# Kernel tuning notes

Measured on AMD Instinct MI355X. Metric: run time of the kernel, lower is better.

The kernel has to match this reference:

```python
import jax, jax.numpy as jnp
import numpy as np

BN_EPS = 1e-5

def _conv1x1(w, b, x):
    # w: (O, C), b: (O,), x: (B, C, T) -> (B, O, T)
    return jnp.einsum('oc,bct->bot', w, x) + b[None, :, None]

def _maxpool2(x):
    # MaxPool1d(kernel_size=2, stride=2): (B, C, T) -> (B, C, T//2)
    B, C, T = x.shape
    return x.reshape(B, C, T // 2, 2).max(axis=-1)

def setup_inputs() -> dict:
    key = jax.random.key(0)
    ks = jax.random.split(key, 11)
    B, C, Ci, T = 4, 256, 128, 8192
    s_in = 1.0 / np.sqrt(C)
    s_ic = 1.0 / np.sqrt(Ci)
    return {
        'x':       jax.random.normal(ks[0], (B, C, T), dtype=jnp.float32),
        'theta_w': jax.random.uniform(ks[1], (Ci, C), jnp.float32, -s_in, s_in),
        'theta_b': jax.random.uniform(ks[2], (Ci,),   jnp.float32, -s_in, s_in),
        'phi_w':   jax.random.uniform(ks[3], (Ci, C), jnp.float32, -s_in, s_in),
        'phi_b':   jax.random.uniform(ks[4], (Ci,),   jnp.float32, -s_in, s_in),
        'g_w':     jax.random.uniform(ks[5], (Ci, C), jnp.float32, -s_in, s_in),
        'g_b':     jax.random.uniform(ks[6], (Ci,),   jnp.float32, -s_in, s_in),
        'w_w':     jax.random.uniform(ks[7], (C, Ci), jnp.float32, -s_ic, s_ic),
        'w_b':     jax.random.uniform(ks[8], (C,),    jnp.float32, -s_ic, s_ic),
        'gamma':   jax.random.normal(ks[9], (C,), dtype=jnp.float32),
        'beta':    jax.random.normal(ks[10], (C,), dtype=jnp.float32),
    }

def reference(x, theta_w, theta_b, phi_w, phi_b, g_w, g_b, w_w, w_b, gamma, beta):
    # x: (B, C, T)
    theta = _conv1x1(theta_w, theta_b, x)            # (B, Ci, T)
    phi   = _maxpool2(_conv1x1(phi_w, phi_b, x))     # (B, Ci, N), N = T//2
    g     = _maxpool2(_conv1x1(g_w, g_b, x))         # (B, Ci, N)
    N = phi.shape[-1]
    # f = theta^T phi / N  (dot-product similarity, divide-by-N normalization)
    f = jnp.einsum('bct,bcn->btn', theta, phi) / N   # (B, T, N)
    y = jnp.einsum('btn,bcn->bct', f, g)             # (B, Ci, T)
    wy = _conv1x1(w_w, w_b, y)                       # (B, C, T)
    # BatchNorm1d (training mode: batch statistics over (B, T), biased var)
    mean = wy.mean(axis=(0, 2), keepdims=True)
    var = ((wy - mean) ** 2).mean(axis=(0, 2), keepdims=True)
    bn = gamma[None, :, None] * (wy - mean) * jax.lax.rsqrt(var + BN_EPS) + beta[None, :, None]
    return bn + x
```

## Files before the change

kernel.cpp:

```cpp
#include <hip/hip_runtime.h>
#include <hip/hip_bf16.h>


constexpr int B = 4, C = 256, CI = 128, T = 8192, NN = 4096;

using s16x8 = __attribute__((ext_vector_type(8))) short;
using f32x4 = __attribute__((ext_vector_type(4))) float;

__device__ __forceinline__ unsigned short f2bf(float f) {
    unsigned int x = __float_as_uint(f);
    unsigned int r = (x + 0x7fffu + ((x >> 16) & 1u)) >> 16;
    return (unsigned short)r;
}
__device__ __forceinline__ float bf2f(unsigned short u) {
    return __uint_as_float((unsigned int)u << 16);
}

#define MFMA(a, b, c) __builtin_amdgcn_mfma_f32_16x16x32_bf16((a), (b), (c), 0, 0, 0)

constexpr size_t SZ_XT = (size_t)B * T * C * 2;
constexpr size_t O_XTH = 0;
constexpr size_t O_XTL = O_XTH + SZ_XT;
constexpr size_t O_WSH = O_XTL + SZ_XT;
constexpr size_t O_WSL = O_WSH + (size_t)C * C * 2;
constexpr size_t SZ_P  = (size_t)B * CI * NN * 2;
constexpr size_t O_PH  = O_WSL + (size_t)C * C * 2;
constexpr size_t O_PL  = O_PH + SZ_P;
constexpr size_t O_GH  = O_PL + SZ_P;
constexpr size_t O_GL  = O_GH + SZ_P;
constexpr size_t O_S   = O_GL + SZ_P;
constexpr size_t O_M   = O_S  + (size_t)B * CI * CI * 4;
constexpr size_t O_W2H = O_M  + (size_t)B * C * CI * 4;
constexpr size_t O_W2L = O_W2H + (size_t)B * C * C * 2;
constexpr size_t O_B2  = O_W2L + (size_t)B * C * C * 2;
constexpr size_t O_GS  = O_B2 + (size_t)B * C * 4;
constexpr size_t O_GQ  = O_GS + (size_t)C * 4;
constexpr size_t O_A   = O_GQ + (size_t)C * 4;
constexpr size_t O_SH  = O_A  + (size_t)C * 4;

__global__ __launch_bounds__(256) void k0_split(
    const float* __restrict__ x, unsigned short* __restrict__ xth,
    unsigned short* __restrict__ xtl)
{
    __shared__ float xs[64][65];
    int t0 = blockIdx.x * 64, c0 = blockIdx.y * 64, b = blockIdx.z;
    int tid = threadIdx.x;
    const float* xb = x + (size_t)b * C * T;
    #pragma unroll
    for (int p = 0; p < 4; ++p) {
        int idx = tid + p * 256;
        int cr = idx >> 4;
        int tg = (idx & 15) * 4;
        float4 v = *reinterpret_cast<const float4*>(xb + (size_t)(c0 + cr) * T + t0 + tg);
        xs[tg + 0][cr] = v.x; xs[tg + 1][cr] = v.y;
        xs[tg + 2][cr] = v.z; xs[tg + 3][cr] = v.w;
    }
    __syncthreads();
    #pragma unroll
    for (int p = 0; p < 2; ++p) {
        int idx = tid + p * 256;
        int cg = idx & 7, tl = idx >> 3;
        s16x8 hs, ls;
        #pragma unroll
        for (int j = 0; j < 8; ++j) {
            float v = xs[tl][cg * 8 + j];
            unsigned short h = f2bf(v);
            unsigned short l = f2bf(v - bf2f(h));
            hs[j] = (short)h; ls[j] = (short)l;
        }
        size_t dst = ((size_t)b * T + t0 + tl) * C + c0 + cg * 8;
        *reinterpret_cast<s16x8*>(xth + dst) = hs;
        *reinterpret_cast<s16x8*>(xtl + dst) = ls;
    }
}

__global__ __launch_bounds__(256) void k0w(
    const float* __restrict__ phi_w, const float* __restrict__ g_w,
    unsigned short* __restrict__ wsh, unsigned short* __restrict__ wsl)
{
    int idx = blockIdx.x * 256 + threadIdx.x;
    int row = idx >> 8, c = idx & 255;
    float v = (row < CI) ? phi_w[(size_t)row * C + c] : g_w[(size_t)(row - CI) * C + c];
    unsigned short h = f2bf(v);
    wsh[idx] = h;
    wsl[idx] = f2bf(v - bf2f(h));
}

__global__ __launch_bounds__(512) void k1_mfma(
    const unsigned short* __restrict__ xth, const unsigned short* __restrict__ xtl,
    const unsigned short* __restrict__ wsh, const unsigned short* __restrict__ wsl,
    const float* __restrict__ phi_b, const float* __restrict__ g_b,
    unsigned short* __restrict__ ph, unsigned short* __restrict__ pl,
    unsigned short* __restrict__ gh, unsigned short* __restrict__ gl)
{
    int b = blockIdx.y, t0 = blockIdx.x * 128;
    int tid = threadIdx.x, lane = tid & 63, w = tid >> 6;
    int wo = w & 3, th = w >> 2;
    int lr = lane & 15, lk = lane >> 4;

    f32x4 acc[4][4];
    #pragma unroll
    for (int i = 0; i < 4; ++i)
        #pragma unroll
        for (int j = 0; j < 4; ++j) acc[i][j] = (f32x4){0.f, 0.f, 0.f, 0.f};

    const unsigned short* ah_b = xth + ((size_t)b * T + t0 + th * 64 + lr) * C + lk * 8;
    const unsigned short* al_b = xtl + ((size_t)b * T + t0 + th * 64 + lr) * C + lk * 8;
    const unsigned short* bh_b = wsh + (size_t)(wo * 64 + lr) * C + lk * 8;
    const unsigned short* bl_b = wsl + (size_t)(wo * 64 + lr) * C + lk * 8;

    for (int c0 = 0; c0 < C; c0 += 32) {
        s16x8 Ah[4], Al[4], Bh[4], Bl[4];
        #pragma unroll
        for (int ts = 0; ts < 4; ++ts) {
            Ah[ts] = *reinterpret_cast<const s16x8*>(ah_b + (size_t)ts * 16 * C + c0);
            Al[ts] = *reinterpret_cast<const s16x8*>(al_b + (size_t)ts * 16 * C + c0);
        }
        #pragma unroll
        for (int os = 0; os < 4; ++os) {
            Bh[os] = *reinterpret_cast<const s16x8*>(bh_b + (size_t)os * 16 * C + c0);
            Bl[os] = *reinterpret_cast<const s16x8*>(bl_b + (size_t)os * 16 * C + c0);
        }
        #pragma unroll
        for (int os = 0; os < 4; ++os)
            #pragma unroll
            for (int ts = 0; ts < 4; ++ts) {
                acc[os][ts] = MFMA(Ah[ts], Bh[os], acc[os][ts]);
                acc[os][ts] = MFMA(Al[ts], Bh[os], acc[os][ts]);
                acc[os][ts] = MFMA(Ah[ts], Bl[os], acc[os][ts]);
            }
    }

    __shared__ unsigned int pool_s[256][65];
    #pragma unroll
    for (int os = 0; os < 4; ++os) {
        int o = wo * 64 + os * 16 + lr;
        float bias = (o < CI) ? phi_b[o] : g_b[o - CI];
        #pragma unroll
        for (int ts = 0; ts < 4; ++ts) {
            f32x4 v = acc[os][ts];
            float m0 = fmaxf(v[0], v[1]) + bias;
            float m1 = fmaxf(v[2], v[3]) + bias;
            int nl = th * 32 + ts * 8 + lk * 2;
            unsigned short h0 = f2bf(m0), h1 = f2bf(m1);
            unsigned int u0 = (unsigned int)h0 | ((unsigned int)f2bf(m0 - bf2f(h0)) << 16);
            unsigned int u1 = (unsigned int)h1 | ((unsigned int)f2bf(m1 - bf2f(h1)) << 16);
            pool_s[o][nl] = u0;
            pool_s[o][nl + 1] = u1;
        }
    }
    __syncthreads();
    int o = tid >> 1, hf = tid & 1;
    size_t n0 = (size_t)(t0 >> 1) + hf * 32;
    unsigned short* dh = (o < CI ? ph + ((size_t)b * CI + o) * NN
                                 : gh + ((size_t)b * CI + o - CI) * NN) + n0;
    unsigned short* dl = (o < CI ? pl + ((size_t)b * CI + o) * NN
                                 : gl + ((size_t)b * CI + o - CI) * NN) + n0;
    #pragma unroll
    for (int g4 = 0; g4 < 4; ++g4) {
        s16x8 hs, ls;
        #pragma unroll
        for (int j = 0; j < 8; ++j) {
            unsigned int u = pool_s[o][hf * 32 + g4 * 8 + j];
            hs[j] = (short)(u & 0xffffu);
            ls[j] = (short)(u >> 16);
        }
        *reinterpret_cast<s16x8*>(dh + g4 * 8) = hs;
        *reinterpret_cast<s16x8*>(dl + g4 * 8) = ls;
    }
}

__global__ __launch_bounds__(256) void k2_mfma(
    const unsigned short* __restrict__ ph, const unsigned short* __restrict__ pl,
    const unsigned short* __restrict__ gh, const unsigned short* __restrict__ gl,
    float* __restrict__ S)
{
    int b = blockIdx.y, n0 = blockIdx.x * 512;
    int tid = threadIdx.x, lane = tid & 63, w = tid >> 6;
    int lr = lane & 15, lk = lane >> 4;

    f32x4 acc[2][8];
    #pragma unroll
    for (int i = 0; i < 2; ++i)
        #pragma unroll
        for (int j = 0; j < 8; ++j) acc[i][j] = (f32x4){0.f, 0.f, 0.f, 0.f};

    const unsigned short* ah_b = gh + ((size_t)b * CI + w * 32 + lr) * NN + n0 + lk * 8;
    const unsigned short* al_b = gl + ((size_t)b * CI + w * 32 + lr) * NN + n0 + lk * 8;
    const unsigned short* bh_b = ph + ((size_t)b * CI + lr) * NN + n0 + lk * 8;
    const unsigned short* bl_b = pl + ((size_t)b * CI + lr) * NN + n0 + lk * 8;

    for (int ks = 0; ks < 16; ++ks) {
        s16x8 Ah[2], Al[2], Bh[8], Bl[8];
        #pragma unroll
        for (int is = 0; is < 2; ++is) {
            Ah[is] = *reinterpret_cast<const s16x8*>(ah_b + (size_t)is * 16 * NN + ks * 32);
            Al[is] = *reinterpret_cast<const s16x8*>(al_b + (size_t)is * 16 * NN + ks * 32);
        }
        #pragma unroll
        for (int js = 0; js < 8; ++js) {
            Bh[js] = *reinterpret_cast<const s16x8*>(bh_b + (size_t)js * 16 * NN + ks * 32);
            Bl[js] = *reinterpret_cast<const s16x8*>(bl_b + (size_t)js * 16 * NN + ks * 32);
        }
        #pragma unroll
        for (int is = 0; is < 2; ++is)
            #pragma unroll
            for (int js = 0; js < 8; ++js) {
                acc[is][js] = MFMA(Ah[is], Bh[js], acc[is][js]);
                acc[is][js] = MFMA(Al[is], Bh[js], acc[is][js]);
                acc[is][js] = MFMA(Ah[is], Bl[js], acc[is][js]);
            }
    }
    #pragma unroll
    for (int is = 0; is < 2; ++is) {
        int i0 = w * 32 + is * 16 + lk * 4;
        #pragma unroll
        for (int js = 0; js < 8; ++js) {
            int j = js * 16 + lr;
            #pragma unroll
            for (int r = 0; r < 4; ++r)
                atomicAdd(&S[((size_t)b * CI + i0 + r) * CI + j], acc[is][js][r]);
        }
    }
}

__global__ __launch_bounds__(256) void k3a_M(
    const float* __restrict__ w_w, const float* __restrict__ S, float* __restrict__ M)
{
    int idx = blockIdx.x * 256 + threadIdx.x;
    int j = idx & (CI - 1);
    int r = (idx >> 7) & (C - 1);
    int b = idx >> 15;
    const float* Sb = S + (size_t)b * CI * CI;
    float a = 0.f;
    for (int k = 0; k < CI; ++k) a += w_w[(size_t)r * CI + k] * Sb[(size_t)k * CI + j];
    M[idx] = a * (1.f / NN);
}

__global__ __launch_bounds__(256) void k3b_W2(
    const float* __restrict__ M, const float* __restrict__ theta_w,
    const float* __restrict__ theta_b, const float* __restrict__ w_b,
    unsigned short* __restrict__ w2h, unsigned short* __restrict__ w2l,
    float* __restrict__ b2)
{
    int idx = blockIdx.x * 256 + threadIdx.x;
    int c = idx & (C - 1);
    int r = (idx >> 8) & (C - 1);
    int b = idx >> 16;
    const float* Mb = M + ((size_t)b * C + r) * CI;
    float a = 0.f;
    for (int k = 0; k < CI; ++k) a += Mb[k] * theta_w[(size_t)k * C + c];
    unsigned short h = f2bf(a);
    w2h[idx] = h;
    w2l[idx] = f2bf(a - bf2f(h));
    if (c == 0) {
        float bv = 0.f;
        for (int k = 0; k < CI; ++k) bv += Mb[k] * theta_b[k];
        b2[(size_t)b * C + r] = bv + w_b[r];
    }
}

template <int MODE>
__global__ __launch_bounds__(512) void k45_mfma(
    const unsigned short* __restrict__ xth, const unsigned short* __restrict__ xtl,
    const unsigned short* __restrict__ w2h, const unsigned short* __restrict__ w2l,
    const float* __restrict__ b2, const float* __restrict__ x,
    const float* __restrict__ abuf, const float* __restrict__ shbuf,
    float* __restrict__ gsum, float* __restrict__ gsq, float* __restrict__ out)
{
    int b = blockIdx.y, t0 = blockIdx.x * 128;
    int tid = threadIdx.x, lane = tid & 63, w = tid >> 6;
    int wo = w & 3, th = w >> 2;
    int lr = lane & 15, lk = lane >> 4;

    f32x4 acc[4][4];
    #pragma unroll
    for (int i = 0; i < 4; ++i)
        #pragma unroll
        for (int j = 0; j < 4; ++j) acc[i][j] = (f32x4){0.f, 0.f, 0.f, 0.f};

    const unsigned short* ah_b = xth + ((size_t)b * T + t0 + th * 64 + lr) * C + lk * 8;
    const unsigned short* al_b = xtl + ((size_t)b * T + t0 + th * 64 + lr) * C + lk * 8;
    const unsigned short* bh_b = w2h + (size_t)b * C * C + (size_t)(wo * 64 + lr) * C + lk * 8;
    const unsigned short* bl_b = w2l + (size_t)b * C * C + (size_t)(wo * 64 + lr) * C + lk * 8;

    for (int c0 = 0; c0 < C; c0 += 32) {
        s16x8 Ah[4], Al[4], Bh[4], Bl[4];
        #pragma unroll
        for (int ts = 0; ts < 4; ++ts) {
            Ah[ts] = *reinterpret_cast<const s16x8*>(ah_b + (size_t)ts * 16 * C + c0);
            Al[ts] = *reinterpret_cast<const s16x8*>(al_b + (size_t)ts * 16 * C + c0);
        }
        #pragma unroll
        for (int os = 0; os < 4; ++os) {
            Bh[os] = *reinterpret_cast<const s16x8*>(bh_b + (size_t)os * 16 * C + c0);
            Bl[os] = *reinterpret_cast<const s16x8*>(bl_b + (size_t)os * 16 * C + c0);
        }
        #pragma unroll
        for (int os = 0; os < 4; ++os)
            #pragma unroll
            for (int ts = 0; ts < 4; ++ts) {
                acc[os][ts] = MFMA(Ah[ts], Bh[os], acc[os][ts]);
                acc[os][ts] = MFMA(Al[ts], Bh[os], acc[os][ts]);
                acc[os][ts] = MFMA(Ah[ts], Bl[os], acc[os][ts]);
            }
    }

    #pragma unroll
    for (int os = 0; os < 4; ++os) {
        int o = wo * 64 + os * 16 + lr;
        float bv = b2[(size_t)b * C + o];
        if (MODE == 0) {
            float s = 0.f, q = 0.f;
            #pragma unroll
            for (int ts = 0; ts < 4; ++ts)
                #pragma unroll
                for (int r = 0; r < 4; ++r) {
                    float v = acc[os][ts][r] + bv;
                    s += v; q += v * v;
                }
            s += __shfl_xor(s, 16); s += __shfl_xor(s, 32);
            q += __shfl_xor(q, 16); q += __shfl_xor(q, 32);
            if (lk == 0) { atomicAdd(&gsum[o], s); atomicAdd(&gsq[o], q); }
        } else {
            float av = abuf[o], sv = shbuf[o];
            #pragma unroll
            for (int ts = 0; ts < 4; ++ts) {
                int t = t0 + th * 64 + ts * 16 + lk * 4;
                size_t base = ((size_t)b * C + o) * T + t;
                float4 xv = *reinterpret_cast<const float4*>(x + base);
                float4 ov;
                ov.x = av * (acc[os][ts][0] + bv) + sv + xv.x;
                ov.y = av * (acc[os][ts][1] + bv) + sv + xv.y;
                ov.z = av * (acc[os][ts][2] + bv) + sv + xv.z;
                ov.w = av * (acc[os][ts][3] + bv) + sv + xv.w;
                *reinterpret_cast<float4*>(out + base) = ov;
            }
        }
    }
}

__global__ void k4b_stats(const float* __restrict__ gsum, const float* __restrict__ gsq,
                          const float* __restrict__ gamma, const float* __restrict__ beta,
                          float* __restrict__ a, float* __restrict__ sh)
{
    int c = threadIdx.x;
    const float invBT = 1.f / (float)(B * T);
    float mean = gsum[c] * invBT;
    float var  = gsq[c] * invBT - mean * mean;
    float av = gamma[c] * rsqrtf(var + 1e-5f);
    a[c]  = av;
    sh[c] = beta[c] - av * mean;
}

extern "C" void kernel_launch(void* const* d_in, const int* in_sizes, int n_in,
                              void* d_out, int out_size, void* d_ws, size_t ws_size,
                              hipStream_t stream)
{
    const float* x       = (const float*)d_in[0];
    const float* theta_w = (const float*)d_in[1];
    const float* theta_b = (const float*)d_in[2];
    const float* phi_w   = (const float*)d_in[3];
    const float* phi_b   = (const float*)d_in[4];
    const float* g_w     = (const float*)d_in[5];
    const float* g_b     = (const float*)d_in[6];
    const float* w_w     = (const float*)d_in[7];
    const float* w_b     = (const float*)d_in[8];
    const float* gamma   = (const float*)d_in[9];
    const float* beta    = (const float*)d_in[10];
    float* out = (float*)d_out;
    char* ws = (char*)d_ws;

    unsigned short* xth = (unsigned short*)(ws + O_XTH);
    unsigned short* xtl = (unsigned short*)(ws + O_XTL);
    unsigned short* wsh = (unsigned short*)(ws + O_WSH);
    unsigned short* wsl = (unsigned short*)(ws + O_WSL);
    unsigned short* ph  = (unsigned short*)(ws + O_PH);
    unsigned short* pl  = (unsigned short*)(ws + O_PL);
    unsigned short* gh  = (unsigned short*)(ws + O_GH);
    unsigned short* gl  = (unsigned short*)(ws + O_GL);
    float* Sbuf  = (float*)(ws + O_S);
    float* Mbuf  = (float*)(ws + O_M);
    unsigned short* w2h = (unsigned short*)(ws + O_W2H);
    unsigned short* w2l = (unsigned short*)(ws + O_W2L);
    float* b2    = (float*)(ws + O_B2);
    float* gsum  = (float*)(ws + O_GS);
    float* gsq   = (float*)(ws + O_GQ);
    float* abuf  = (float*)(ws + O_A);
    float* shbuf = (float*)(ws + O_SH);

    hipMemsetAsync(Sbuf, 0, (size_t)B * CI * CI * sizeof(float), stream);
    hipMemsetAsync(gsum, 0, 2 * (size_t)C * sizeof(float), stream);

    k0_split<<<dim3(T / 64, C / 64, B), 256, 0, stream>>>(x, xth, xtl);
    k0w<<<dim3(C * C / 256), 256, 0, stream>>>(phi_w, g_w, wsh, wsl);
    k1_mfma<<<dim3(T / 128, B), 512, 0, stream>>>(xth, xtl, wsh, wsl, phi_b, g_b,
                                                  ph, pl, gh, gl);
    k2_mfma<<<dim3(NN / 512, B), 256, 0, stream>>>(ph, pl, gh, gl, Sbuf);
    k3a_M<<<dim3(B * C * CI / 256), 256, 0, stream>>>(w_w, Sbuf, Mbuf);
    k3b_W2<<<dim3(B * C * C / 256), 256, 0, stream>>>(Mbuf, theta_w, theta_b, w_b,
                                                      w2h, w2l, b2);
    k45_mfma<0><<<dim3(T / 128, B), 512, 0, stream>>>(xth, xtl, w2h, w2l, b2, x,
                                                      abuf, shbuf, gsum, gsq, out);
    k4b_stats<<<1, C, 0, stream>>>(gsum, gsq, gamma, beta, abuf, shbuf);
    k45_mfma<1><<<dim3(T / 128, B), 512, 0, stream>>>(xth, xtl, w2h, w2l, b2, x,
                                                      abuf, shbuf, gsum, gsq, out);
}
```

Baseline: 284.2 us.

## Split output channels across blocks and double-buffer register loads in MFMA GEMMs

Result: slower. 333.9 us (+17.5%).

```diff
diff --git a/kernel.cpp b/kernel.cpp
--- a/kernel.cpp
+++ b/kernel.cpp
@@ -86,6 +86,43 @@
     wsl[idx] = f2bf(v - bf2f(h));
 }
 
+#define LD_SET(ah, al, bh, bl, c0)                                            \
+    {                                                                          \
+        _Pragma("unroll")                                                      \
+        for (int ts_ = 0; ts_ < 2; ++ts_) {                                    \
+            ah[ts_] = *reinterpret_cast<const s16x8*>(aBaseH + (size_t)ts_ * 16 * C + (c0)); \
+            al[ts_] = *reinterpret_cast<const s16x8*>(aBaseL + (size_t)ts_ * 16 * C + (c0)); \
+        }                                                                      \
+        _Pragma("unroll")                                                      \
+        for (int os_ = 0; os_ < 4; ++os_) {                                    \
+            bh[os_] = *reinterpret_cast<const s16x8*>(bBaseH + (size_t)os_ * 16 * C + (c0)); \
+            bl[os_] = *reinterpret_cast<const s16x8*>(bBaseL + (size_t)os_ * 16 * C + (c0)); \
+        }                                                                      \
+    }
+
+#define MM_SET(ah, al, bh, bl)                                                 \
+    {                                                                          \
+        _Pragma("unroll")                                                      \
+        for (int os_ = 0; os_ < 4; ++os_)                                      \
+            _Pragma("unroll")                                                  \
+            for (int ts_ = 0; ts_ < 2; ++ts_) {                                \
+                acc[os_][ts_] = MFMA(ah[ts_], bh[os_], acc[os_][ts_]);         \
+                acc[os_][ts_] = MFMA(al[ts_], bh[os_], acc[os_][ts_]);         \
+                acc[os_][ts_] = MFMA(ah[ts_], bl[os_], acc[os_][ts_]);         \
+            }                                                                  \
+    }
+
+#define GEMM_CORE()                                                            \
+    s16x8 a0h[2], a0l[2], b0h[4], b0l[4];                                      \
+    s16x8 a1h[2], a1l[2], b1h[4], b1l[4];                                      \
+    LD_SET(a0h, a0l, b0h, b0l, 0)                                              \
+    for (int kk = 0; kk < C; kk += 64) {                                       \
+        LD_SET(a1h, a1l, b1h, b1l, kk + 32)                                    \
+        MM_SET(a0h, a0l, b0h, b0l)                                             \
+        if (kk + 64 < C) LD_SET(a0h, a0l, b0h, b0l, kk + 64)                   \
+        MM_SET(a1h, a1l, b1h, b1l)                                             \
+    }
+
 __global__ __launch_bounds__(512) void k1_mfma(
     const unsigned short* __restrict__ xth, const unsigned short* __restrict__ xtl,
     const unsigned short* __restrict__ wsh, const unsigned short* __restrict__ wsl,
@@ -93,75 +130,54 @@
     unsigned short* __restrict__ ph, unsigned short* __restrict__ pl,
     unsigned short* __restrict__ gh, unsigned short* __restrict__ gl)
 {
-    int b = blockIdx.y, t0 = blockIdx.x * 128;
-    int tid = threadIdx.x, lane = tid & 63, w = tid >> 6;
-    int wo = w & 3, th = w >> 2;
-    int lr = lane & 15, lk = lane >> 4;
-
-    f32x4 acc[4][4];
+    const int b = blockIdx.z, t0 = blockIdx.x * 128;
+    const int isG = blockIdx.y;
+    const int o0 = isG * 128;
+    const int tid = threadIdx.x, lane = tid & 63, w = tid >> 6;
+    const int wo = w & 1, th = w >> 1;
+    const int lr = lane & 15, lk = lane >> 4;
+
+    f32x4 acc[4][2];
     #pragma unroll
     for (int i = 0; i < 4; ++i)
         #pragma unroll
-        for (int j = 0; j < 4; ++j) acc[i][j] = (f32x4){0.f, 0.f, 0.f, 0.f};
-
-    const unsigned short* ah_b = xth + ((size_t)b * T + t0 + th * 64 + lr) * C + lk * 8;
-    const unsigned short* al_b = xtl + ((size_t)b * T + t0 + th * 64 + lr) * C + lk * 8;
-    const unsigned short* bh_b = wsh + (size_t)(wo * 64 + lr) * C + lk * 8;
-    const unsigned short* bl_b = wsl + (size_t)(wo * 64 + lr) * C + lk * 8;
-
-    for (int c0 = 0; c0 < C; c0 += 32) {
-        s16x8 Ah[4], Al[4], Bh[4], Bl[4];
-        #pragma unroll
-        for (int ts = 0; ts < 4; ++ts) {
-            Ah[ts] = *reinterpret_cast<const s16x8*>(ah_b + (size_t)ts * 16 * C + c0);
-            Al[ts] = *reinterpret_cast<const s16x8*>(al_b + (size_t)ts * 16 * C + c0);
-        }
-        #pragma unroll
-        for (int os = 0; os < 4; ++os) {
-            Bh[os] = *reinterpret_cast<const s16x8*>(bh_b + (size_t)os * 16 * C + c0);
-            Bl[os] = *reinterpret_cast<const s16x8*>(bl_b + (size_t)os * 16 * C + c0);
-        }
-        #pragma unroll
-        for (int os = 0; os < 4; ++os)
-            #pragma unroll
-            for (int ts = 0; ts < 4; ++ts) {
-                acc[os][ts] = MFMA(Ah[ts], Bh[os], acc[os][ts]);
-                acc[os][ts] = MFMA(Al[ts], Bh[os], acc[os][ts]);
-                acc[os][ts] = MFMA(Ah[ts], Bl[os], acc[os][ts]);
-            }
-    }
-
-    __shared__ unsigned int pool_s[256][65];
+        for (int j = 0; j < 2; ++j) acc[i][j] = (f32x4){0.f, 0.f, 0.f, 0.f};
+
+    const unsigned short* aBaseH = xth + ((size_t)b * T + t0 + th * 32 + lr) * C + lk * 8;
+    const unsigned short* aBaseL = xtl + ((size_t)b * T + t0 + th * 32 + lr) * C + lk * 8;
+    const unsigned short* bBaseH = wsh + (size_t)(o0 + wo * 64 + lr) * C + lk * 8;
+    const unsigned short* bBaseL = wsl + (size_t)(o0 + wo * 64 + lr) * C + lk * 8;
+
+    GEMM_CORE()
+
+    __shared__ unsigned int pool_s[128][65];
+    const float* biasArr = isG ? g_b : phi_b;
     #pragma unroll
     for (int os = 0; os < 4; ++os) {
-        int o = wo * 64 + os * 16 + lr;
-        float bias = (o < CI) ? phi_b[o] : g_b[o - CI];
-        #pragma unroll
-        for (int ts = 0; ts < 4; ++ts) {
+        int oL = wo * 64 + os * 16 + lr;
+        float bias = biasArr[oL];
+        #pragma unroll
+        for (int ts = 0; ts < 2; ++ts) {
             f32x4 v = acc[os][ts];
             float m0 = fmaxf(v[0], v[1]) + bias;
             float m1 = fmaxf(v[2], v[3]) + bias;
-            int nl = th * 32 + ts * 8 + lk * 2;
+            int nl = th * 16 + ts * 8 + lk * 2;
             unsigned short h0 = f2bf(m0), h1 = f2bf(m1);
-            unsigned int u0 = (unsigned int)h0 | ((unsigned int)f2bf(m0 - bf2f(h0)) << 16);
-            unsigned int u1 = (unsigned int)h1 | ((unsigned int)f2bf(m1 - bf2f(h1)) << 16);
-            pool_s[o][nl] = u0;
-            pool_s[o][nl + 1] = u1;
+            pool_s[oL][nl]     = (unsigned int)h0 | ((unsigned int)f2bf(m0 - bf2f(h0)) << 16);
+            pool_s[oL][nl + 1] = (unsigned int)h1 | ((unsigned int)f2bf(m1 - bf2f(h1)) << 16);
         }
     }
     __syncthreads();
-    int o = tid >> 1, hf = tid & 1;
-    size_t n0 = (size_t)(t0 >> 1) + hf * 32;
-    unsigned short* dh = (o < CI ? ph + ((size_t)b * CI + o) * NN
-                                 : gh + ((size_t)b * CI + o - CI) * NN) + n0;
-    unsigned short* dl = (o < CI ? pl + ((size_t)b * CI + o) * NN
-                                 : gl + ((size_t)b * CI + o - CI) * NN) + n0;
-    #pragma unroll
-    for (int g4 = 0; g4 < 4; ++g4) {
+    int oL = tid >> 2, seg = tid & 3;
+    size_t n0 = (size_t)(t0 >> 1) + seg * 16;
+    unsigned short* dh = (isG ? gh : ph) + ((size_t)b * CI + oL) * NN + n0;
+    unsigned short* dl = (isG ? gl : pl) + ((size_t)b * CI + oL) * NN + n0;
+    #pragma unroll
+    for (int g4 = 0; g4 < 2; ++g4) {
         s16x8 hs, ls;
         #pragma unroll
         for (int j = 0; j < 8; ++j) {
-            unsigned int u = pool_s[o][hf * 32 + g4 * 8 + j];
+            unsigned int u = pool_s[oL][seg * 16 + g4 * 8 + j];
             hs[j] = (short)(u & 0xffffu);
             ls[j] = (short)(u >> 16);
         }
@@ -268,52 +284,32 @@
     const float* __restrict__ abuf, const float* __restrict__ shbuf,
     float* __restrict__ gsum, float* __restrict__ gsq, float* __restrict__ out)
 {
-    int b = blockIdx.y, t0 = blockIdx.x * 128;
-    int tid = threadIdx.x, lane = tid & 63, w = tid >> 6;
-    int wo = w & 3, th = w >> 2;
-    int lr = lane & 15, lk = lane >> 4;
-
-    f32x4 acc[4][4];
+    const int b = blockIdx.z, t0 = blockIdx.x * 128, o0 = blockIdx.y * 128;
+    const int tid = threadIdx.x, lane = tid & 63, w = tid >> 6;
+    const int wo = w & 1, th = w >> 1;
+    const int lr = lane & 15, lk = lane >> 4;
+
+    f32x4 acc[4][2];
     #pragma unroll
     for (int i = 0; i < 4; ++i)
         #pragma unroll
-        for (int j = 0; j < 4; ++j) acc[i][j] = (f32x4){0.f, 0.f, 0.f, 0.f};
-
-    const unsigned short* ah_b = xth + ((size_t)b * T + t0 + th * 64 + lr) * C + lk * 8;
-    const unsigned short* al_b = xtl + ((size_t)b * T + t0 + th * 64 + lr) * C + lk * 8;
-    const unsigned short* bh_b = w2h + (size_t)b * C * C + (size_t)(wo * 64 + lr) * C + lk * 8;
-    const unsigned short* bl_b = w2l + (size_t)b * C * C + (size_t)(wo * 64 + lr) * C + lk * 8;
-
-    for (int c0 = 0; c0 < C; c0 += 32) {
-        s16x8 Ah[4], Al[4], Bh[4], Bl[4];
-        #pragma unroll
-        for (int ts = 0; ts < 4; ++ts) {
-            Ah[ts] = *reinterpret_cast<const s16x8*>(ah_b + (size_t)ts * 16 * C + c0);
-            Al[ts] = *reinterpret_cast<const s16x8*>(al_b + (size_t)ts * 16 * C + c0);
-        }
-        #pragma unroll
-        for (int os = 0; os < 4; ++os) {
-            Bh[os] = *reinterpret_cast<const s16x8*>(bh_b + (size_t)os * 16 * C + c0);
-            Bl[os] = *reinterpret_cast<const s16x8*>(bl_b + (size_t)os * 16 * C + c0);
-        }
-        #pragma unroll
-        for (int os = 0; os < 4; ++os)
-            #pragma unroll
-            for (int ts = 0; ts < 4; ++ts) {
-                acc[os][ts] = MFMA(Ah[ts], Bh[os], acc[os][ts]);
-                acc[os][ts] = MFMA(Al[ts], Bh[os], acc[os][ts]);
-                acc[os][ts] = MFMA(Ah[ts], Bl[os], acc[os][ts]);
-            }
-    }
+        for (int j = 0; j < 2; ++j) acc[i][j] = (f32x4){0.f, 0.f, 0.f, 0.f};
+
+    const unsigned short* aBaseH = xth + ((size_t)b * T + t0 + th * 32 + lr) * C + lk * 8;
+    const unsigned short* aBaseL = xtl + ((size_t)b * T + t0 + th * 32 + lr) * C + lk * 8;
+    const unsigned short* bBaseH = w2h + (size_t)b * C * C + (size_t)(o0 + wo * 64 + lr) * C + lk * 8;
+    const unsigned short* bBaseL = w2l + (size_t)b * C * C + (size_t)(o0 + wo * 64 + lr) * C + lk * 8;
+
+    GEMM_CORE()
 
     #pragma unroll
     for (int os = 0; os < 4; ++os) {
-        int o = wo * 64 + os * 16 + lr;
+        int o = o0 + wo * 64 + os * 16 + lr;
         float bv = b2[(size_t)b * C + o];
         if (MODE == 0) {
             float s = 0.f, q = 0.f;
             #pragma unroll
-            for (int ts = 0; ts < 4; ++ts)
+            for (int ts = 0; ts < 2; ++ts)
                 #pragma unroll
                 for (int r = 0; r < 4; ++r) {
                     float v = acc[os][ts][r] + bv;
@@ -325,8 +321,8 @@
         } else {
             float av = abuf[o], sv = shbuf[o];
             #pragma unroll
-            for (int ts = 0; ts < 4; ++ts) {
-                int t = t0 + th * 64 + ts * 16 + lk * 4;
+            for (int ts = 0; ts < 2; ++ts) {
+                int t = t0 + th * 32 + ts * 16 + lk * 4;
                 size_t base = ((size_t)b * C + o) * T + t;
                 float4 xv = *reinterpret_cast<const float4*>(x + base);
                 float4 ov;
@@ -394,15 +390,15 @@
 
     k0_split<<<dim3(T / 64, C / 64, B), 256, 0, stream>>>(x, xth, xtl);
     k0w<<<dim3(C * C / 256), 256, 0, stream>>>(phi_w, g_w, wsh, wsl);
-    k1_mfma<<<dim3(T / 128, B), 512, 0, stream>>>(xth, xtl, wsh, wsl, phi_b, g_b,
-                                                  ph, pl, gh, gl);
+    k1_mfma<<<dim3(T / 128, 2, B), 512, 0, stream>>>(xth, xtl, wsh, wsl, phi_b, g_b,
+                                                     ph, pl, gh, gl);
     k2_mfma<<<dim3(NN / 512, B), 256, 0, stream>>>(ph, pl, gh, gl, Sbuf);
     k3a_M<<<dim3(B * C * CI / 256), 256, 0, stream>>>(w_w, Sbuf, Mbuf);
     k3b_W2<<<dim3(B * C * C / 256), 256, 0, stream>>>(Mbuf, theta_w, theta_b, w_b,
                                                       w2h, w2l, b2);
-    k45_mfma<0><<<dim3(T / 128, B), 512, 0, stream>>>(xth, xtl, w2h, w2l, b2, x,
-                                                      abuf, shbuf, gsum, gsq, out);
+    k45_mfma<0><<<dim3(T / 128, C / 128, B), 512, 0, stream>>>(
+        xth, xtl, w2h, w2l, b2, x, abuf, shbuf, gsum, gsq, out);
     k4b_stats<<<1, C, 0, stream>>>(gsum, gsq, gamma, beta, abuf, shbuf);
-    k45_mfma<1><<<dim3(T / 128, B), 512, 0, stream>>>(xth, xtl, w2h, w2l, b2, x,
-                                                      abuf, shbuf, gsum, gsq, out);
-}
+    k45_mfma<1><<<dim3(T / 128, C / 128, B), 512, 0, stream>>>(
+        xth, xtl, w2h, w2l, b2, x, abuf, shbuf, gsum, gsq, out);
+}
```
